# Kernel optimization log

Measured on AMD Instinct MI355X. Metric: run time of the kernel, lower is better.

The kernel has to match this reference:

```python
import jax, jax.numpy as jnp
import numpy as np

D_MODEL = 1024
D_FFN = 2048
WINDOW = 64
EPS = 1e-6


def rmsnorm(x, w):
    rms = jnp.sqrt(jnp.mean(x * x, axis=-1, keepdims=True) + EPS)
    return x / rms * w


def setup_inputs() -> dict:
    key = jax.random.key(0)
    ks = jax.random.split(key, 9)
    s = 0.02
    return {
        "x": jax.random.normal(ks[0], (4, 2048, D_MODEL), dtype=jnp.float32),
        "norm1_w": jnp.ones((D_MODEL,), dtype=jnp.float32),
        "norm2_w": jnp.ones((D_MODEL,), dtype=jnp.float32),
        "Wq": jax.random.normal(ks[1], (D_MODEL, D_MODEL), dtype=jnp.float32) * s,
        "Wk": jax.random.normal(ks[2], (D_MODEL, D_MODEL), dtype=jnp.float32) * s,
        "Wv": jax.random.normal(ks[3], (D_MODEL, D_MODEL), dtype=jnp.float32) * s,
        "Wo": jax.random.normal(ks[4], (D_MODEL, D_MODEL), dtype=jnp.float32) * s,
        "W1": jax.random.normal(ks[5], (D_MODEL, D_FFN), dtype=jnp.float32) * s,
        "W2": jax.random.normal(ks[6], (D_FFN, D_MODEL), dtype=jnp.float32) * s,
        "W3": jax.random.normal(ks[7], (D_MODEL, D_FFN), dtype=jnp.float32) * s,
    }


def reference(x, norm1_w, norm2_w, Wq, Wk, Wv, Wo, W1, W2, W3):
    B, T, D = x.shape
    scale = D ** (-0.5)
    residual = x
    xn = rmsnorm(x, norm1_w)
    q = xn @ Wq  # [B,T,D]
    k = xn @ Wk
    v = xn @ Wv
    # causal local-window mask: attend iff 0 <= i-j < WINDOW
    rows = jnp.arange(T)[:, None]
    cols = jnp.arange(T)[None, :]
    mask = (cols <= rows) & (rows - cols < WINDOW)  # [T,T] bool
    scores = jnp.einsum("bid,bjd->bij", q, k) * scale
    scores = jnp.where(mask[None], scores, -jnp.inf)
    weights = jax.nn.softmax(scores, axis=-1)
    attended = jnp.einsum("bij,bjd->bid", weights, v)
    x = residual + attended @ Wo
    # SwiGLU FFN
    xn2 = rmsnorm(x, norm2_w)
    ffn = (jax.nn.silu(xn2 @ W1) * (xn2 @ W3)) @ W2
    return x + ffn
```

## Files before the change

kernel.cpp:

```cpp
#include <hip/hip_runtime.h>
#include <hip/hip_bf16.h>

typedef __attribute__((ext_vector_type(8))) short bf16x8;
typedef __attribute__((ext_vector_type(4))) float f32x4;

__device__ __forceinline__ short to_bf16s(float f) {
    union { __hip_bfloat16 h; short s; } u;
    u.h = __float2bfloat16(f);
    return u.s;
}

__device__ __forceinline__ void load_lds16(const void* g, void* l) {
    __builtin_amdgcn_global_load_lds((const __attribute__((address_space(1))) void*)g,
                                     (__attribute__((address_space(3))) void*)l, 16, 0, 0);
}

__global__ __launch_bounds__(256)
void prep_kernel(const float* __restrict__ Wq, const float* __restrict__ Wk,
                 const float* __restrict__ Wv, const float* __restrict__ Wo,
                 const float* __restrict__ W1, const float* __restrict__ W3,
                 const float* __restrict__ W2,
                 short* __restrict__ WqT, short* __restrict__ WkT,
                 short* __restrict__ WvT, short* __restrict__ WoT,
                 short* __restrict__ W13T, short* __restrict__ W2T,
                 const float* __restrict__ x, const float* __restrict__ n1w,
                 short* __restrict__ xn1) {
    const int bid = blockIdx.x;
    const int t = threadIdx.x;
    if (bid >= 10240) {
        const long row = bid - 10240;
        float4 v = ((const float4*)(x + row * 1024))[t];
        float ss = v.x * v.x + v.y * v.y + v.z * v.z + v.w * v.w;
        #pragma unroll
        for (int off = 32; off; off >>= 1) ss += __shfl_xor(ss, off);
        __shared__ float red[4];
        if ((t & 63) == 0) red[t >> 6] = ss;
        __syncthreads();
        ss = red[0] + red[1] + red[2] + red[3];
        const float inv = rsqrtf(ss * (1.0f / 1024.0f) + 1e-6f);
        float4 wv = ((const float4*)n1w)[t];
        short4 o;
        o.x = to_bf16s(v.x * inv * wv.x);
        o.y = to_bf16s(v.y * inv * wv.y);
        o.z = to_bf16s(v.z * inv * wv.z);
        o.w = to_bf16s(v.w * inv * wv.w);
        *(short4*)&xn1[row * 1024 + t * 4] = o;
        return;
    }
    __shared__ float tile[32][33];
    const float* src; short* dst; int K, N, tl, rs = 1, ro = 0;
    if (bid < 4096) {
        const int wi = bid >> 10; tl = bid & 1023;
        src = wi == 0 ? Wq : wi == 1 ? Wk : wi == 2 ? Wv : Wo;
        dst = wi == 0 ? WqT : wi == 1 ? WkT : wi == 2 ? WvT : WoT;
        K = 1024; N = 1024;
    } else if (bid < 8192) {
        const int wi = (bid - 4096) >> 11; tl = (bid - 4096) & 2047;
        src = wi ? W3 : W1; dst = W13T; rs = 2; ro = wi;
        K = 1024; N = 2048;
    } else {
        tl = bid - 8192; src = W2; dst = W2T;
        K = 2048; N = 1024;
    }
    const int nx = N >> 5;
    const int n0 = (tl % nx) * 32, k0 = (tl / nx) * 32;
    {
        const int lr = t >> 3, lc = (t & 7) * 4;
        float4 v = *(const float4*)&src[(long)(k0 + lr) * N + n0 + lc];
        tile[lr][lc] = v.x; tile[lr][lc + 1] = v.y;
        tile[lr][lc + 2] = v.z; tile[lr][lc + 3] = v.w;
    }
    __syncthreads();
    {
        const int nr = t >> 3, kc = (t & 7) * 4;
        short4 o;
        o.x = to_bf16s(tile[kc][nr]);
        o.y = to_bf16s(tile[kc + 1][nr]);
        o.z = to_bf16s(tile[kc + 2][nr]);
        o.w = to_bf16s(tile[kc + 3][nr]);
        *(short4*)&dst[(long)((n0 + nr) * rs + ro) * K + k0 + kc] = o;
    }
}

__global__ __launch_bounds__(256)
void rmsnorm_kernel(const float* __restrict__ x, const float* __restrict__ wt,
                    short* __restrict__ out) {
    const long row = blockIdx.x;
    const int t = threadIdx.x;
    float4 v = ((const float4*)(x + row * 1024))[t];
    float ss = v.x * v.x + v.y * v.y + v.z * v.z + v.w * v.w;
    #pragma unroll
    for (int off = 32; off; off >>= 1) ss += __shfl_xor(ss, off);
    __shared__ float red[4];
    if ((t & 63) == 0) red[t >> 6] = ss;
    __syncthreads();
    ss = red[0] + red[1] + red[2] + red[3];
    const float inv = rsqrtf(ss * (1.0f / 1024.0f) + 1e-6f);
    float4 wv = ((const float4*)wt)[t];
    short4 o;
    o.x = to_bf16s(v.x * inv * wv.x);
    o.y = to_bf16s(v.y * inv * wv.y);
    o.z = to_bf16s(v.z * inv * wv.z);
    o.w = to_bf16s(v.w * inv * wv.w);
    *(short4*)&out[row * 1024 + t * 4] = o;
}

#define MFMA16(MB, NB, BREG)                                                   \
    __builtin_amdgcn_s_barrier();                                              \
    asm volatile("s_waitcnt lgkmcnt(0)");                                      \
    __builtin_amdgcn_s_setprio(1);                                             \
    _Pragma("unroll")                                                          \
    for (int m_ = 0; m_ < 4; ++m_)                                             \
        _Pragma("unroll")                                                      \
        for (int n_ = 0; n_ < 2; ++n_) {                                       \
            acc[(MB) + m_][(NB) + n_] = __builtin_amdgcn_mfma_f32_16x16x32_bf16( \
                a[m_][0], BREG[n_][0], acc[(MB) + m_][(NB) + n_], 0, 0, 0);    \
            acc[(MB) + m_][(NB) + n_] = __builtin_amdgcn_mfma_f32_16x16x32_bf16( \
                a[m_][1], BREG[n_][1], acc[(MB) + m_][(NB) + n_], 0, 0, 0);    \
        }                                                                      \
    __builtin_amdgcn_s_setprio(0);                                             \
    __builtin_amdgcn_s_barrier();

#define QRA(BUF)                                                               \
    _Pragma("unroll")                                                          \
    for (int m_ = 0; m_ < 4; ++m_) {                                           \
        const int rb_ = ((BUF) * 2 + (wr >> 1)) * 16384 +                      \
                        ((wr & 1) * 64 + m_ * 16 + lm) * 128;                  \
        a[m_][0] = *(const bf16x8*)&lds[rb_ + ((lk * 16) ^ sw)];               \
        a[m_][1] = *(const bf16x8*)&lds[rb_ + ((64 + lk * 16) ^ sw)];          \
    }
#define QRB(BUF, NG, ARR)                                                      \
    _Pragma("unroll")                                                          \
    for (int n_ = 0; n_ < 2; ++n_) {                                           \
        const int rb_ = 65536 + ((BUF) * 2 + wc) * 8192 +                      \
                        (((NG) * 2 + n_) * 16 + lm) * 128;                     \
        ARR[n_][0] = *(const bf16x8*)&lds[rb_ + ((lk * 16) ^ sw)];             \
        ARR[n_][1] = *(const bf16x8*)&lds[rb_ + ((64 + lk * 16) ^ sw)];        \
    }

__global__ __launch_bounds__(512, 2)
void gemm256qkv(const short* __restrict__ A, const short* __restrict__ B0,
                short* __restrict__ outp, short* __restrict__ outp2,
                int M, int N, int K) {
    __shared__ __align__(16) char lds[98304];

    const int t = threadIdx.x;
    const int lane = t & 63, w = t >> 6;
    const int wr = w >> 1, wc = w & 1;
    const int lm = lane & 15, lk = lane >> 4;
    const int sw = (lm & 7) << 4;

    const int nbn = N >> 7;
    const int chunk = gridDim.x >> 3;
    const int logical = (blockIdx.x & 7) * chunk + (blockIdx.x >> 3);
    const int bm = logical / nbn, bn = logical - (logical / nbn) * nbn;

    const long Kb = (long)K * 2;
    const char* Ab = (const char*)A;
    const char* Bb = (const char*)B0;

    long srcA[2][2], srcB[2];
    {
        const int rowp = t >> 3;
        const int cbx = (t & 7) * 16;
        const int swz = ((t >> 3) & 7) << 4;
        #pragma unroll
        for (int h = 0; h < 2; ++h)
            #pragma unroll
            for (int c = 0; c < 2; ++c)
                srcA[h][c] = (long)(bm * 256 + h * 128 + c * 64 + rowp) * Kb + (cbx ^ swz);
        #pragma unroll
        for (int h = 0; h < 2; ++h)
            srcB[h] = (long)(bn * 128 + h * 64 + rowp) * Kb + (cbx ^ swz);
    }
    auto stA = [&](int kt, int h) {
        const int buf = kt & 1;
        #pragma unroll
        for (int c = 0; c < 2; ++c)
            load_lds16(Ab + srcA[h][c] + (long)kt * 128,
                       &lds[(buf * 2 + h) * 16384 + c * 8192 + t * 16]);
    };
    auto stB = [&](int kt, int h) {
        const int buf = kt & 1;
        load_lds16(Bb + srcB[h] + (long)kt * 128,
                   &lds[65536 + (buf * 2 + h) * 8192 + t * 16]);
    };

    f32x4 acc[4][4] = {};
    bf16x8 a[4][2], b0[2][2], b1[2][2];
    const int nt = K >> 6;

    stA(0, 0); stA(0, 1); stB(0, 0); stB(0, 1);
    stA(1, 0); stA(1, 1); stB(1, 0); stB(1, 1);
    asm volatile("s_waitcnt vmcnt(6)" ::: "memory");
    __builtin_amdgcn_s_barrier();

    for (int u = 0; u < nt; u += 2) {
        const bool pf = (u + 2) < nt;
        QRA(0); QRB(0, 0, b0);
        if (pf) stA(u + 2, 0);
        MFMA16(0, 0, b0)
        QRB(0, 1, b1);
        if (pf) { stA(u + 2, 1); stB(u + 2, 0); stB(u + 2, 1);
                  asm volatile("s_waitcnt vmcnt(6)" ::: "memory"); }
        else    { asm volatile("s_waitcnt vmcnt(0)" ::: "memory"); }
        MFMA16(0, 2, b1)
        QRA(1); QRB(1, 0, b0);
        if (pf) stA(u + 3, 0);
        MFMA16(0, 0, b0)
        QRB(1, 1, b1);
        if (pf) { stA(u + 3, 1); stB(u + 3, 0); stB(u + 3, 1);
                  asm volatile("s_waitcnt vmcnt(6)" ::: "memory"); }
        else    { asm volatile("s_waitcnt vmcnt(0)" ::: "memory"); }
        MFMA16(0, 2, b1)
    }

    #pragma unroll
    for (int mf = 0; mf < 4; ++mf)
      #pragma unroll
      for (int nf = 0; nf < 4; ++nf)
        #pragma unroll
        for (int r = 0; r < 4; ++r) {
            const int grow = bm * 256 + wr * 64 + mf * 16 + lk * 4 + r;
            const int gcol = bn * 128 + wc * 64 + nf * 16 + lm;
            const float v = acc[mf][nf][r];
            if (gcol < 2048)
                outp[(long)grow * 2048 + gcol] = to_bf16s(v);
            else
                outp2[(long)(gcol - 2048) * 8192 + grow] = to_bf16s(v);
        }
}

__global__ __launch_bounds__(256, 2)
void gemm128o(const short* __restrict__ A, const short* __restrict__ B0,
              const float* __restrict__ res, float* __restrict__ outp,
              int M, int N, int K) {
    __shared__ __align__(16) char lds[65536];

    const int t = threadIdx.x;
    const int lane = t & 63, w = t >> 6;
    const int wr = w >> 1, wc = w & 1;
    const int lm = lane & 15, lk = lane >> 4;
    const int sw = (lm & 7) << 4;

    const int nbn = N >> 7;
    const int chunk = gridDim.x >> 3;
    const int logical = (blockIdx.x & 7) * chunk + (blockIdx.x >> 3);
    const int bm = logical / nbn, bn = logical - (logical / nbn) * nbn;

    const long Kb = (long)K * 2;
    const char* Ab = (const char*)A;
    const char* Bb = (const char*)B0;

    long srcA[4], srcB[4];
    {
        const int rowp = t >> 3;
        const int cbx = (t & 7) * 16;
        const int swz = ((t >> 3) & 7) << 4;
        #pragma unroll
        for (int c = 0; c < 4; ++c) {
            srcA[c] = (long)(bm * 128 + c * 32 + rowp) * Kb + (cbx ^ swz);
            srcB[c] = (long)(bn * 128 + c * 32 + rowp) * Kb + (cbx ^ swz);
        }
    }
    auto stage = [&](int kt, int buf) {
        #pragma unroll
        for (int c = 0; c < 4; ++c)
            load_lds16(Ab + srcA[c] + (long)kt * 128,
                       &lds[buf * 16384 + c * 4096 + t * 16]);
        #pragma unroll
        for (int c = 0; c < 4; ++c)
            load_lds16(Bb + srcB[c] + (long)kt * 128,
                       &lds[32768 + buf * 16384 + c * 4096 + t * 16]);
    };

    f32x4 acc[4][4] = {};
    const int nt = K >> 6;

    stage(0, 0);
    asm volatile("s_waitcnt vmcnt(0)" ::: "memory");
    __syncthreads();

    for (int kt = 0; kt < nt; ++kt) {
        const int buf = kt & 1;
        if (kt + 1 < nt) stage(kt + 1, buf ^ 1);
        bf16x8 a[4][2], b[4][2];
        #pragma unroll
        for (int m = 0; m < 4; ++m) {
            const int rb = buf * 16384 + (wr * 64 + m * 16 + lm) * 128;
            a[m][0] = *(const bf16x8*)&lds[rb + ((lk * 16) ^ sw)];
            a[m][1] = *(const bf16x8*)&lds[rb + ((64 + lk * 16) ^ sw)];
        }
        #pragma unroll
        for (int n = 0; n < 4; ++n) {
            const int rb = 32768 + buf * 16384 + (wc * 64 + n * 16 + lm) * 128;
            b[n][0] = *(const bf16x8*)&lds[rb + ((lk * 16) ^ sw)];
            b[n][1] = *(const bf16x8*)&lds[rb + ((64 + lk * 16) ^ sw)];
        }
        #pragma unroll
        for (int m = 0; m < 4; ++m)
            #pragma unroll
            for (int n = 0; n < 4; ++n) {
                acc[m][n] = __builtin_amdgcn_mfma_f32_16x16x32_bf16(a[m][0], b[n][0], acc[m][n], 0, 0, 0);
                acc[m][n] = __builtin_amdgcn_mfma_f32_16x16x32_bf16(a[m][1], b[n][1], acc[m][n], 0, 0, 0);
            }
        __syncthreads();
    }

    #pragma unroll
    for (int m = 0; m < 4; ++m)
      #pragma unroll
      for (int n = 0; n < 4; ++n)
        #pragma unroll
        for (int r = 0; r < 4; ++r) {
            const int grow = bm * 128 + wr * 64 + m * 16 + lk * 4 + r;
            const int gcol = bn * 128 + wc * 64 + n * 16 + lm;
            const long i = (long)grow * N + gcol;
            outp[i] = res[i] + acc[m][n][r];
        }
}

#define RA2(BUF, MG)                                                           \
    _Pragma("unroll")                                                          \
    for (int m_ = 0; m_ < 4; ++m_) {                                           \
        const int rb_ = ((BUF) * 2 + wr) * 16384 + (((MG) * 4 + m_) * 16 + lm) * 128; \
        a[m_][0] = *(const bf16x8*)&lds[rb_ + ((lk * 16) ^ sw)];               \
        a[m_][1] = *(const bf16x8*)&lds[rb_ + ((64 + lk * 16) ^ sw)];          \
    }
#define RB2(BUF, NH, ARR)                                                      \
    _Pragma("unroll")                                                          \
    for (int n_ = 0; n_ < 2; ++n_) {                                           \
        const int rb_ = 65536 + ((BUF) * 2 + (wc >> 1)) * 16384 +              \
                        ((wc & 1) * 64 + ((NH) * 2 + n_) * 16 + lm) * 128;     \
        ARR[n_][0] = *(const bf16x8*)&lds[rb_ + ((lk * 16) ^ sw)];             \
        ARR[n_][1] = *(const bf16x8*)&lds[rb_ + ((64 + lk * 16) ^ sw)];        \
    }

__global__ __launch_bounds__(512, 2)
void gemm256f(const short* __restrict__ A, const short* __restrict__ B0,
              short* __restrict__ outp, int M, int N, int K) {
    __shared__ __align__(16) char lds[131072];

    const int t = threadIdx.x;
    const int lane = t & 63, w = t >> 6;
    const int wr = w >> 2, wc = w & 3;
    const int lm = lane & 15, lk = lane >> 4;
    const int sw = (lm & 7) << 4;

    const int nbn = N >> 8;
    const int chunk = gridDim.x >> 3;
    const int logical = (blockIdx.x & 7) * chunk + (blockIdx.x >> 3);
    const int bm = logical / nbn, bn = logical - (logical / nbn) * nbn;

    const long Kb = (long)K * 2;
    const char* Ab = (const char*)A;
    const char* Bb = (const char*)B0;

    long srcA[2][2], srcB[2][2];
    {
        const int rowp = t >> 3;
        const int cbx = (t & 7) * 16;
        const int swz = ((t >> 3) & 7) << 4;
        #pragma unroll
        for (int h = 0; h < 2; ++h)
            #pragma unroll
            for (int c = 0; c < 2; ++c) {
                srcA[h][c] = (long)(bm * 256 + h * 128 + c * 64 + rowp) * Kb + (cbx ^ swz);
                srcB[h][c] = (long)(bn * 256 + h * 128 + c * 64 + rowp) * Kb + (cbx ^ swz);
            }
    }
    auto stA = [&](int kt, int h) {
        const int buf = kt & 1;
        #pragma unroll
        for (int c = 0; c < 2; ++c)
            load_lds16(Ab + srcA[h][c] + (long)kt * 128,
                       &lds[(buf * 2 + h) * 16384 + c * 8192 + t * 16]);
    };
    auto stB = [&](int kt, int h) {
        const int buf = kt & 1;
        #pragma unroll
        for (int c = 0; c < 2; ++c)
            load_lds16(Bb + srcB[h][c] + (long)kt * 128,
                       &lds[65536 + (buf * 2 + h) * 16384 + c * 8192 + t * 16]);
    };

    f32x4 acc[8][4] = {};
    bf16x8 a[4][2], b0[2][2], b1[2][2];
    const int nt = K >> 6;

    stB(0, 0); stB(0, 1); stA(0, 0); stA(0, 1); stB(1, 0); stB(1, 1);
    asm volatile("s_waitcnt vmcnt(4)" ::: "memory");
    __builtin_amdgcn_s_barrier();

    for (int u = 0; u < nt; u += 2) {
        const bool pf = (u + 2) < nt;
        RA2(0, 0); RB2(0, 0, b0);
        stA(u + 1, 0);
        MFMA16(0, 0, b0)
        RB2(0, 1, b1);
        stA(u + 1, 1);
        MFMA16(0, 2, b1)
        RA2(0, 1);
        if (pf) stB(u + 2, 0);
        MFMA16(4, 2, b1)
        if (pf) { stB(u + 2, 1); asm volatile("s_waitcnt vmcnt(4)" ::: "memory"); }
        else    { asm volatile("s_waitcnt vmcnt(0)" ::: "memory"); }
        MFMA16(4, 0, b0)
        RA2(1, 0); RB2(1, 0, b0);
        if (pf) stA(u + 2, 0);
        MFMA16(0, 0, b0)
        RB2(1, 1, b1);
        if (pf) stA(u + 2, 1);
        MFMA16(0, 2, b1)
        RA2(1, 1);
        if (pf) stB(u + 3, 0);
        MFMA16(4, 2, b1)
        if (pf) { stB(u + 3, 1); asm volatile("s_waitcnt vmcnt(4)" ::: "memory"); }
        else    { asm volatile("s_waitcnt vmcnt(0)" ::: "memory"); }
        MFMA16(4, 0, b0)
    }

    const int NH = N >> 1;
    #pragma unroll
    for (int mf = 0; mf < 8; ++mf)
      #pragma unroll
      for (int nf = 0; nf < 4; ++nf)
        #pragma unroll
        for (int r = 0; r < 4; ++r) {
            const int grow = bm * 256 + wr * 128 + mf * 16 + lk * 4 + r;
            const int gcol = bn * 256 + wc * 64 + nf * 16 + lm;
            const float v = acc[mf][nf][r];
            const float g3 = __shfl_xor(v, 1);
            if (!(lane & 1)) {
                const float sws = v / (1.f + __expf(-v));
                outp[(long)grow * NH + (gcol >> 1)] = to_bf16s(sws * g3);
            }
        }
}

__global__ __launch_bounds__(128)
void attn_kernel(const short* __restrict__ Q, const short* __restrict__ Km,
                 int ldq, const short* __restrict__ VT, short* __restrict__ att) {
    const int T = 2048, D = 1024, Mtot = 8192;
    const int bid = blockIdx.x;
    const int b = bid >> 6;
    const int q0 = (bid & 63) << 5;
    const long qrow0 = (long)b * T + q0;
    const int t = threadIdx.x, lane = t & 63, w = t >> 6;

    __shared__ short Qs[2][32 * 32];
    __shared__ short Ks[2][96 * 32];
    __shared__ float S_lds[32][100];
    __shared__ short P_lds[32 * 96];
    __shared__ short VTs[2][128 * 96];

    const int trow = t >> 2, tk8 = (t & 3) * 8;
    auto stageQK = [&](int kt, int bf) {
        const int k0 = kt << 5;
        load_lds16(Q + (qrow0 + trow) * ldq + k0 + tk8, &Qs[bf][t * 8]);
        #pragma unroll
        for (int s2 = 0; s2 < 3; ++s2) {
            const int krow = s2 * 32 + trow;
            int j = q0 - 64 + krow; if (j < 0) j = 0;
            load_lds16(Km + ((long)b * T + j) * ldq + k0 + tk8, &Ks[bf][(s2 * 128 + t) * 8]);
        }
    };

    f32x4 s[6] = {};
    stageQK(0, 0);
    __syncthreads();
    for (int kt = 0; kt < 32; ++kt) {
        const int cb = kt & 1;
        if (kt + 1 < 32) stageQK(kt + 1, cb ^ 1);
        const int ko = (lane >> 4) * 8;
        const bf16x8 aq = *(const bf16x8*)&Qs[cb][(w * 16 + (lane & 15)) * 32 + ko];
        #pragma unroll
        for (int n = 0; n < 6; ++n) {
            const bf16x8 bk = *(const bf16x8*)&Ks[cb][(n * 16 + (lane & 15)) * 32 + ko];
            s[n] = __builtin_amdgcn_mfma_f32_16x16x32_bf16(aq, bk, s[n], 0, 0, 0);
        }
        __syncthreads();
    }
    #pragma unroll
    for (int n = 0; n < 6; ++n)
        #pragma unroll
        for (int r = 0; r < 4; ++r)
            S_lds[w * 16 + ((lane >> 4) << 2) + r][n * 16 + (lane & 15)] = s[n][r] * 0.03125f;
    __syncthreads();

    {
        const int row = t >> 2, c0 = (t & 3) * 24;
        float e[24];
        float mx = -1e30f;
        #pragma unroll
        for (int c = 0; c < 24; ++c) {
            const int kj = c0 + c;
            const bool valid = (kj > row) && (kj <= row + 64) && (q0 - 64 + kj >= 0);
            const float sv = valid ? S_lds[row][kj] : -1e30f;
            e[c] = sv;
            mx = fmaxf(mx, sv);
        }
        mx = fmaxf(mx, __shfl_xor(mx, 1));
        mx = fmaxf(mx, __shfl_xor(mx, 2));
        float sum = 0.f;
        #pragma unroll
        for (int c = 0; c < 24; ++c) {
            const float ev = (e[c] > -1e29f) ? __expf(e[c] - mx) : 0.f;
            e[c] = ev; sum += ev;
        }
        sum += __shfl_xor(sum, 1);
        sum += __shfl_xor(sum, 2);
        const float inv = 1.f / sum;
        #pragma unroll
        for (int c = 0; c < 24; ++c)
            P_lds[row * 96 + c0 + c] = to_bf16s(e[c] * inv);
    }

    auto stageV = [&](int dc, int bf) {
        #pragma unroll
        for (int s2 = 0; s2 < 12; ++s2) {
            const int idx = s2 * 128 + t;
            const int dr = idx / 12, c = idx - dr * 12;
            int j = q0 - 64 + c * 8; if (j < 0) j = 0;
            load_lds16(VT + (long)(dc * 128 + dr) * Mtot + b * T + j, &VTs[bf][idx * 8]);
        }
    };
    stageV(0, 0);
    __syncthreads();

    bf16x8 pa[3];
    {
        const int ko = (lane >> 4) * 8;
        #pragma unroll
        for (int kc = 0; kc < 3; ++kc)
            pa[kc] = *(const bf16x8*)&P_lds[(w * 16 + (lane & 15)) * 96 + kc * 32 + ko];
    }
    for (int dc = 0; dc < 8; ++dc) {
        const int cb = dc & 1;
        if (dc + 1 < 8) stageV(dc + 1, cb ^ 1);
        f32x4 o[8] = {};
        const int ko = (lane >> 4) * 8;
        #pragma unroll
        for (int kc = 0; kc < 3; ++kc)
            #pragma unroll
            for (int n = 0; n < 8; ++n) {
                const bf16x8 vb = *(const bf16x8*)&VTs[cb][(n * 16 + (lane & 15)) * 96 + kc * 32 + ko];
                o[n] = __builtin_amdgcn_mfma_f32_16x16x32_bf16(pa[kc], vb, o[n], 0, 0, 0);
            }
        __syncthreads();
        #pragma unroll
        for (int n = 0; n < 8; ++n)
            #pragma unroll
            for (int r = 0; r < 4; ++r) {
                const long grow = qrow0 + w * 16 + ((lane >> 4) << 2) + r;
                const int gcol = dc * 128 + n * 16 + (lane & 15);
                att[grow * D + gcol] = to_bf16s(o[n][r]);
            }
    }
}

extern "C" void kernel_launch(void* const* d_in, const int* in_sizes, int n_in,
                              void* d_out, int out_size, void* d_ws, size_t ws_size,
                              hipStream_t stream) {
    const float* x   = (const float*)d_in[0];
    const float* n1w = (const float*)d_in[1];
    const float* n2w = (const float*)d_in[2];
    const float* Wq  = (const float*)d_in[3];
    const float* Wk  = (const float*)d_in[4];
    const float* Wv  = (const float*)d_in[5];
    const float* Wo  = (const float*)d_in[6];
    const float* W1  = (const float*)d_in[7];
    const float* W2  = (const float*)d_in[8];
    const float* W3  = (const float*)d_in[9];

    const int M = 8192;
    char* ws = (char*)d_ws;
    size_t off = 0;
    auto alloc = [&](size_t bytes) { void* p = ws + off; off += (bytes + 255) & ~(size_t)255; return p; };

    short* xn1 = (short*)alloc((size_t)M * 1024 * 2);
    short* qk  = (short*)alloc((size_t)M * 2048 * 2);
    short* vT  = (short*)alloc((size_t)M * 1024 * 2);
    float* x2  = (float*)alloc((size_t)M * 1024 * 4);
    short* WqT = (short*)alloc((size_t)1024 * 1024 * 2);
    short* WkT = (short*)alloc((size_t)1024 * 1024 * 2);
    short* WvT = (short*)alloc((size_t)1024 * 1024 * 2);
    short* WoT = (short*)alloc((size_t)1024 * 1024 * 2);
    short* W13T= (short*)alloc((size_t)4096 * 1024 * 2);
    short* W2T = (short*)alloc((size_t)1024 * 2048 * 2);
    short* att = xn1;
    short* xn2 = qk;
    short* h   = qk + (size_t)M * 1024;

    prep_kernel<<<18432, 256, 0, stream>>>(Wq, Wk, Wv, Wo, W1, W3, W2,
                                           WqT, WkT, WvT, WoT, W13T, W2T,
                                           x, n1w, xn1);
    gemm256qkv<<<768, 512, 0, stream>>>(xn1, WqT, qk, vT, M, 3072, 1024);
    attn_kernel<<<256, 128, 0, stream>>>(qk, qk + 1024, 2048, vT, att);
    gemm128o<<<512, 256, 0, stream>>>(att, WoT, x, x2, M, 1024, 1024);
    rmsnorm_kernel<<<M, 256, 0, stream>>>(x2, n2w, xn2);
    gemm256f<<<512, 512, 0, stream>>>(xn2, W13T, h, M, 4096, 1024);
    gemm128o<<<512, 256, 0, stream>>>(h, W2T, x2, (float*)d_out, M, 1024, 2048);
}
```

Measured before the change: 299.2 us.

## Retile all GEMMs with simpler single-barrier double-buffered loops and larger tiles

The QKV GEMM moves to 256x192 tiles with 8 waves in a 2x4 layout, giving 512 blocks instead of 768. The two residual GEMMs move from 128x128 tiles with 256 threads to 256x128 tiles with 512 threads. The SwiGLU GEMM and all the others drop the hand-interleaved half-step MFMA/prefetch schedule for a plain per-k-tile double-buffer loop with one barrier and a full vmcnt(0) wait. Larger tiles raise data reuse and cut block count, but the simpler schedule may overlap loads with MFMA less well, and the grids may leave some CUs idle.

```diff
diff --git a/kernel.cpp b/kernel.cpp
--- a/kernel.cpp
+++ b/kernel.cpp
@@ -105,52 +105,20 @@
     *(short4*)&out[row * 1024 + t * 4] = o;
 }
 
-#define MFMA16(MB, NB, BREG)                                                   \
-    __builtin_amdgcn_s_barrier();                                              \
-    asm volatile("s_waitcnt lgkmcnt(0)");                                      \
-    __builtin_amdgcn_s_setprio(1);                                             \
-    _Pragma("unroll")                                                          \
-    for (int m_ = 0; m_ < 4; ++m_)                                             \
-        _Pragma("unroll")                                                      \
-        for (int n_ = 0; n_ < 2; ++n_) {                                       \
-            acc[(MB) + m_][(NB) + n_] = __builtin_amdgcn_mfma_f32_16x16x32_bf16( \
-                a[m_][0], BREG[n_][0], acc[(MB) + m_][(NB) + n_], 0, 0, 0);    \
-            acc[(MB) + m_][(NB) + n_] = __builtin_amdgcn_mfma_f32_16x16x32_bf16( \
-                a[m_][1], BREG[n_][1], acc[(MB) + m_][(NB) + n_], 0, 0, 0);    \
-        }                                                                      \
-    __builtin_amdgcn_s_setprio(0);                                             \
-    __builtin_amdgcn_s_barrier();
-
-#define QRA(BUF)                                                               \
-    _Pragma("unroll")                                                          \
-    for (int m_ = 0; m_ < 4; ++m_) {                                           \
-        const int rb_ = ((BUF) * 2 + (wr >> 1)) * 16384 +                      \
-                        ((wr & 1) * 64 + m_ * 16 + lm) * 128;                  \
-        a[m_][0] = *(const bf16x8*)&lds[rb_ + ((lk * 16) ^ sw)];               \
-        a[m_][1] = *(const bf16x8*)&lds[rb_ + ((64 + lk * 16) ^ sw)];          \
-    }
-#define QRB(BUF, NG, ARR)                                                      \
-    _Pragma("unroll")                                                          \
-    for (int n_ = 0; n_ < 2; ++n_) {                                           \
-        const int rb_ = 65536 + ((BUF) * 2 + wc) * 8192 +                      \
-                        (((NG) * 2 + n_) * 16 + lm) * 128;                     \
-        ARR[n_][0] = *(const bf16x8*)&lds[rb_ + ((lk * 16) ^ sw)];             \
-        ARR[n_][1] = *(const bf16x8*)&lds[rb_ + ((64 + lk * 16) ^ sw)];        \
-    }
 
 __global__ __launch_bounds__(512, 2)
-void gemm256qkv(const short* __restrict__ A, const short* __restrict__ B0,
+void gemm192qkv(const short* __restrict__ A, const short* __restrict__ B0,
                 short* __restrict__ outp, short* __restrict__ outp2,
                 int M, int N, int K) {
-    __shared__ __align__(16) char lds[98304];
+    __shared__ __align__(16) char lds[114688];
 
     const int t = threadIdx.x;
     const int lane = t & 63, w = t >> 6;
-    const int wr = w >> 1, wc = w & 1;
+    const int wr = w >> 2, wc = w & 3;
     const int lm = lane & 15, lk = lane >> 4;
     const int sw = (lm & 7) << 4;
 
-    const int nbn = N >> 7;
+    const int nbn = N / 192;
     const int chunk = gridDim.x >> 3;
     const int logical = (blockIdx.x & 7) * chunk + (blockIdx.x >> 3);
     const int bm = logical / nbn, bn = logical - (logical / nbn) * nbn;
@@ -159,70 +127,88 @@
     const char* Ab = (const char*)A;
     const char* Bb = (const char*)B0;
 
-    long srcA[2][2], srcB[2];
+    long srcA[4], srcB[3];
     {
         const int rowp = t >> 3;
         const int cbx = (t & 7) * 16;
         const int swz = ((t >> 3) & 7) << 4;
         #pragma unroll
-        for (int h = 0; h < 2; ++h)
-            #pragma unroll
-            for (int c = 0; c < 2; ++c)
-                srcA[h][c] = (long)(bm * 256 + h * 128 + c * 64 + rowp) * Kb + (cbx ^ swz);
-        #pragma unroll
-        for (int h = 0; h < 2; ++h)
-            srcB[h] = (long)(bn * 128 + h * 64 + rowp) * Kb + (cbx ^ swz);
-    }
-    auto stA = [&](int kt, int h) {
+        for (int c = 0; c < 4; ++c)
+            srcA[c] = (long)(bm * 256 + c * 64 + rowp) * Kb + (cbx ^ swz);
+        #pragma unroll
+        for (int c = 0; c < 3; ++c)
+            srcB[c] = (long)(bn * 192 + c * 64 + rowp) * Kb + (cbx ^ swz);
+    }
+    auto stage = [&](int kt) {
         const int buf = kt & 1;
         #pragma unroll
-        for (int c = 0; c < 2; ++c)
-            load_lds16(Ab + srcA[h][c] + (long)kt * 128,
-                       &lds[(buf * 2 + h) * 16384 + c * 8192 + t * 16]);
+        for (int c = 0; c < 4; ++c)
+            load_lds16(Ab + srcA[c] + (long)kt * 128, &lds[buf * 32768 + c * 8192 + t * 16]);
+        #pragma unroll
+        for (int c = 0; c < 3; ++c)
+            load_lds16(Bb + srcB[c] + (long)kt * 128, &lds[65536 + buf * 24576 + c * 8192 + t * 16]);
     };
-    auto stB = [&](int kt, int h) {
+
+    f32x4 acc[8][3] = {};
+    bf16x8 a[4][2], b[3][2];
+    const int nt = K >> 6;
+
+    stage(0);
+    asm volatile("s_waitcnt vmcnt(0)" ::: "memory");
+    __builtin_amdgcn_s_barrier();
+
+    for (int kt = 0; kt < nt; ++kt) {
         const int buf = kt & 1;
-        load_lds16(Bb + srcB[h] + (long)kt * 128,
-                   &lds[65536 + (buf * 2 + h) * 8192 + t * 16]);
-    };
-
-    f32x4 acc[4][4] = {};
-    bf16x8 a[4][2], b0[2][2], b1[2][2];
-    const int nt = K >> 6;
-
-    stA(0, 0); stA(0, 1); stB(0, 0); stB(0, 1);
-    stA(1, 0); stA(1, 1); stB(1, 0); stB(1, 1);
-    asm volatile("s_waitcnt vmcnt(6)" ::: "memory");
-    __builtin_amdgcn_s_barrier();
-
-    for (int u = 0; u < nt; u += 2) {
-        const bool pf = (u + 2) < nt;
-        QRA(0); QRB(0, 0, b0);
-        if (pf) stA(u + 2, 0);
-        MFMA16(0, 0, b0)
-        QRB(0, 1, b1);
-        if (pf) { stA(u + 2, 1); stB(u + 2, 0); stB(u + 2, 1);
-                  asm volatile("s_waitcnt vmcnt(6)" ::: "memory"); }
-        else    { asm volatile("s_waitcnt vmcnt(0)" ::: "memory"); }
-        MFMA16(0, 2, b1)
-        QRA(1); QRB(1, 0, b0);
-        if (pf) stA(u + 3, 0);
-        MFMA16(0, 0, b0)
-        QRB(1, 1, b1);
-        if (pf) { stA(u + 3, 1); stB(u + 3, 0); stB(u + 3, 1);
-                  asm volatile("s_waitcnt vmcnt(6)" ::: "memory"); }
-        else    { asm volatile("s_waitcnt vmcnt(0)" ::: "memory"); }
-        MFMA16(0, 2, b1)
+        const bool pf = kt + 1 < nt;
+        #pragma unroll
+        for (int n_ = 0; n_ < 3; ++n_) {
+            const int rb = 65536 + buf * 24576 + (wc * 48 + n_ * 16 + lm) * 128;
+            b[n_][0] = *(const bf16x8*)&lds[rb + ((lk * 16) ^ sw)];
+            b[n_][1] = *(const bf16x8*)&lds[rb + ((64 + lk * 16) ^ sw)];
+        }
+        #pragma unroll
+        for (int m_ = 0; m_ < 4; ++m_) {
+            const int rb = buf * 32768 + (wr * 128 + m_ * 16 + lm) * 128;
+            a[m_][0] = *(const bf16x8*)&lds[rb + ((lk * 16) ^ sw)];
+            a[m_][1] = *(const bf16x8*)&lds[rb + ((64 + lk * 16) ^ sw)];
+        }
+        if (pf) stage(kt + 1);
+        asm volatile("s_waitcnt lgkmcnt(0)");
+        __builtin_amdgcn_s_setprio(1);
+        #pragma unroll
+        for (int m_ = 0; m_ < 4; ++m_)
+            #pragma unroll
+            for (int n_ = 0; n_ < 3; ++n_) {
+                acc[m_][n_] = __builtin_amdgcn_mfma_f32_16x16x32_bf16(a[m_][0], b[n_][0], acc[m_][n_], 0, 0, 0);
+                acc[m_][n_] = __builtin_amdgcn_mfma_f32_16x16x32_bf16(a[m_][1], b[n_][1], acc[m_][n_], 0, 0, 0);
+            }
+        #pragma unroll
+        for (int m_ = 0; m_ < 4; ++m_) {
+            const int rb = buf * 32768 + (wr * 128 + 64 + m_ * 16 + lm) * 128;
+            a[m_][0] = *(const bf16x8*)&lds[rb + ((lk * 16) ^ sw)];
+            a[m_][1] = *(const bf16x8*)&lds[rb + ((64 + lk * 16) ^ sw)];
+        }
+        asm volatile("s_waitcnt lgkmcnt(0)");
+        #pragma unroll
+        for (int m_ = 0; m_ < 4; ++m_)
+            #pragma unroll
+            for (int n_ = 0; n_ < 3; ++n_) {
+                acc[4 + m_][n_] = __builtin_amdgcn_mfma_f32_16x16x32_bf16(a[m_][0], b[n_][0], acc[4 + m_][n_], 0, 0, 0);
+                acc[4 + m_][n_] = __builtin_amdgcn_mfma_f32_16x16x32_bf16(a[m_][1], b[n_][1], acc[4 + m_][n_], 0, 0, 0);
+            }
+        __builtin_amdgcn_s_setprio(0);
+        if (pf) asm volatile("s_waitcnt vmcnt(0)" ::: "memory");
+        __builtin_amdgcn_s_barrier();
     }
 
     #pragma unroll
-    for (int mf = 0; mf < 4; ++mf)
+    for (int mf = 0; mf < 8; ++mf)
       #pragma unroll
-      for (int nf = 0; nf < 4; ++nf)
+      for (int nf = 0; nf < 3; ++nf)
         #pragma unroll
         for (int r = 0; r < 4; ++r) {
-            const int grow = bm * 256 + wr * 64 + mf * 16 + lk * 4 + r;
-            const int gcol = bn * 128 + wc * 64 + nf * 16 + lm;
+            const int grow = bm * 256 + wr * 128 + mf * 16 + lk * 4 + r;
+            const int gcol = bn * 192 + wc * 48 + nf * 16 + lm;
             const float v = acc[mf][nf][r];
             if (gcol < 2048)
                 outp[(long)grow * 2048 + gcol] = to_bf16s(v);
@@ -231,114 +217,9 @@
         }
 }
 
-__global__ __launch_bounds__(256, 2)
-void gemm128o(const short* __restrict__ A, const short* __restrict__ B0,
-              const float* __restrict__ res, float* __restrict__ outp,
-              int M, int N, int K) {
-    __shared__ __align__(16) char lds[65536];
-
-    const int t = threadIdx.x;
-    const int lane = t & 63, w = t >> 6;
-    const int wr = w >> 1, wc = w & 1;
-    const int lm = lane & 15, lk = lane >> 4;
-    const int sw = (lm & 7) << 4;
-
-    const int nbn = N >> 7;
-    const int chunk = gridDim.x >> 3;
-    const int logical = (blockIdx.x & 7) * chunk + (blockIdx.x >> 3);
-    const int bm = logical / nbn, bn = logical - (logical / nbn) * nbn;
-
-    const long Kb = (long)K * 2;
-    const char* Ab = (const char*)A;
-    const char* Bb = (const char*)B0;
-
-    long srcA[4], srcB[4];
-    {
-        const int rowp = t >> 3;
-        const int cbx = (t & 7) * 16;
-        const int swz = ((t >> 3) & 7) << 4;
-        #pragma unroll
-        for (int c = 0; c < 4; ++c) {
-            srcA[c] = (long)(bm * 128 + c * 32 + rowp) * Kb + (cbx ^ swz);
-            srcB[c] = (long)(bn * 128 + c * 32 + rowp) * Kb + (cbx ^ swz);
-        }
-    }
-    auto stage = [&](int kt, int buf) {
-        #pragma unroll
-        for (int c = 0; c < 4; ++c)
-            load_lds16(Ab + srcA[c] + (long)kt * 128,
-                       &lds[buf * 16384 + c * 4096 + t * 16]);
-        #pragma unroll
-        for (int c = 0; c < 4; ++c)
-            load_lds16(Bb + srcB[c] + (long)kt * 128,
-                       &lds[32768 + buf * 16384 + c * 4096 + t * 16]);
-    };
-
-    f32x4 acc[4][4] = {};
-    const int nt = K >> 6;
-
-    stage(0, 0);
-    asm volatile("s_waitcnt vmcnt(0)" ::: "memory");
-    __syncthreads();
-
-    for (int kt = 0; kt < nt; ++kt) {
-        const int buf = kt & 1;
-        if (kt + 1 < nt) stage(kt + 1, buf ^ 1);
-        bf16x8 a[4][2], b[4][2];
-        #pragma unroll
-        for (int m = 0; m < 4; ++m) {
-            const int rb = buf * 16384 + (wr * 64 + m * 16 + lm) * 128;
-            a[m][0] = *(const bf16x8*)&lds[rb + ((lk * 16) ^ sw)];
-            a[m][1] = *(const bf16x8*)&lds[rb + ((64 + lk * 16) ^ sw)];
-        }
-        #pragma unroll
-        for (int n = 0; n < 4; ++n) {
-            const int rb = 32768 + buf * 16384 + (wc * 64 + n * 16 + lm) * 128;
-            b[n][0] = *(const bf16x8*)&lds[rb + ((lk * 16) ^ sw)];
-            b[n][1] = *(const bf16x8*)&lds[rb + ((64 + lk * 16) ^ sw)];
-        }
-        #pragma unroll
-        for (int m = 0; m < 4; ++m)
-            #pragma unroll
-            for (int n = 0; n < 4; ++n) {
-                acc[m][n] = __builtin_amdgcn_mfma_f32_16x16x32_bf16(a[m][0], b[n][0], acc[m][n], 0, 0, 0);
-                acc[m][n] = __builtin_amdgcn_mfma_f32_16x16x32_bf16(a[m][1], b[n][1], acc[m][n], 0, 0, 0);
-            }
-        __syncthreads();
-    }
-
-    #pragma unroll
-    for (int m = 0; m < 4; ++m)
-      #pragma unroll
-      for (int n = 0; n < 4; ++n)
-        #pragma unroll
-        for (int r = 0; r < 4; ++r) {
-            const int grow = bm * 128 + wr * 64 + m * 16 + lk * 4 + r;
-            const int gcol = bn * 128 + wc * 64 + n * 16 + lm;
-            const long i = (long)grow * N + gcol;
-            outp[i] = res[i] + acc[m][n][r];
-        }
-}
-
-#define RA2(BUF, MG)                                                           \
-    _Pragma("unroll")                                                          \
-    for (int m_ = 0; m_ < 4; ++m_) {                                           \
-        const int rb_ = ((BUF) * 2 + wr) * 16384 + (((MG) * 4 + m_) * 16 + lm) * 128; \
-        a[m_][0] = *(const bf16x8*)&lds[rb_ + ((lk * 16) ^ sw)];               \
-        a[m_][1] = *(const bf16x8*)&lds[rb_ + ((64 + lk * 16) ^ sw)];          \
-    }
-#define RB2(BUF, NH, ARR)                                                      \
-    _Pragma("unroll")                                                          \
-    for (int n_ = 0; n_ < 2; ++n_) {                                           \
-        const int rb_ = 65536 + ((BUF) * 2 + (wc >> 1)) * 16384 +              \
-                        ((wc & 1) * 64 + ((NH) * 2 + n_) * 16 + lm) * 128;     \
-        ARR[n_][0] = *(const bf16x8*)&lds[rb_ + ((lk * 16) ^ sw)];             \
-        ARR[n_][1] = *(const bf16x8*)&lds[rb_ + ((64 + lk * 16) ^ sw)];        \
-    }
-
 __global__ __launch_bounds__(512, 2)
-void gemm256f(const short* __restrict__ A, const short* __restrict__ B0,
-              short* __restrict__ outp, int M, int N, int K) {
+void gemm256fv2(const short* __restrict__ A, const short* __restrict__ B0,
+                short* __restrict__ outp, int M, int N, int K) {
     __shared__ __align__(16) char lds[131072];
 
     const int t = threadIdx.x;
@@ -356,68 +237,77 @@
     const char* Ab = (const char*)A;
     const char* Bb = (const char*)B0;
 
-    long srcA[2][2], srcB[2][2];
+    long srcA[4], srcB[4];
     {
         const int rowp = t >> 3;
         const int cbx = (t & 7) * 16;
         const int swz = ((t >> 3) & 7) << 4;
         #pragma unroll
-        for (int h = 0; h < 2; ++h)
-            #pragma unroll
-            for (int c = 0; c < 2; ++c) {
-                srcA[h][c] = (long)(bm * 256 + h * 128 + c * 64 + rowp) * Kb + (cbx ^ swz);
-                srcB[h][c] = (long)(bn * 256 + h * 128 + c * 64 + rowp) * Kb + (cbx ^ swz);
-            }
-    }
-    auto stA = [&](int kt, int h) {
+        for (int c = 0; c < 4; ++c) {
+            srcA[c] = (long)(bm * 256 + c * 64 + rowp) * Kb + (cbx ^ swz);
+            srcB[c] = (long)(bn * 256 + c * 64 + rowp) * Kb + (cbx ^ swz);
+        }
+    }
+    auto stage = [&](int kt) {
         const int buf = kt & 1;
         #pragma unroll
-        for (int c = 0; c < 2; ++c)
-            load_lds16(Ab + srcA[h][c] + (long)kt * 128,
-                       &lds[(buf * 2 + h) * 16384 + c * 8192 + t * 16]);
+        for (int c = 0; c < 4; ++c)
+            load_lds16(Ab + srcA[c] + (long)kt * 128, &lds[buf * 32768 + c * 8192 + t * 16]);
+        #pragma unroll
+        for (int c = 0; c < 4; ++c)
+            load_lds16(Bb + srcB[c] + (long)kt * 128, &lds[65536 + buf * 32768 + c * 8192 + t * 16]);
     };
-    auto stB = [&](int kt, int h) {
+
+    f32x4 acc[8][4] = {};
+    bf16x8 a[4][2], b[4][2];
+    const int nt = K >> 6;
+
+    stage(0);
+    asm volatile("s_waitcnt vmcnt(0)" ::: "memory");
+    __builtin_amdgcn_s_barrier();
+
+    for (int kt = 0; kt < nt; ++kt) {
         const int buf = kt & 1;
-        #pragma unroll
-        for (int c = 0; c < 2; ++c)
-            load_lds16(Bb + srcB[h][c] + (long)kt * 128,
-                       &lds[65536 + (buf * 2 + h) * 16384 + c * 8192 + t * 16]);
-    };
-
-    f32x4 acc[8][4] = {};
-    bf16x8 a[4][2], b0[2][2], b1[2][2];
-    const int nt = K >> 6;
-
-    stB(0, 0); stB(0, 1); stA(0, 0); stA(0, 1); stB(1, 0); stB(1, 1);
-    asm volatile("s_waitcnt vmcnt(4)" ::: "memory");
-    __builtin_amdgcn_s_barrier();
-
-    for (int u = 0; u < nt; u += 2) {
-        const bool pf = (u + 2) < nt;
-        RA2(0, 0); RB2(0, 0, b0);
-        stA(u + 1, 0);
-        MFMA16(0, 0, b0)
-        RB2(0, 1, b1);
-        stA(u + 1, 1);
-        MFMA16(0, 2, b1)
-        RA2(0, 1);
-        if (pf) stB(u + 2, 0);
-        MFMA16(4, 2, b1)
-        if (pf) { stB(u + 2, 1); asm volatile("s_waitcnt vmcnt(4)" ::: "memory"); }
-        else    { asm volatile("s_waitcnt vmcnt(0)" ::: "memory"); }
-        MFMA16(4, 0, b0)
-        RA2(1, 0); RB2(1, 0, b0);
-        if (pf) stA(u + 2, 0);
-        MFMA16(0, 0, b0)
-        RB2(1, 1, b1);
-        if (pf) stA(u + 2, 1);
-        MFMA16(0, 2, b1)
-        RA2(1, 1);
-        if (pf) stB(u + 3, 0);
-        MFMA16(4, 2, b1)
-        if (pf) { stB(u + 3, 1); asm volatile("s_waitcnt vmcnt(4)" ::: "memory"); }
-        else    { asm volatile("s_waitcnt vmcnt(0)" ::: "memory"); }
-        MFMA16(4, 0, b0)
+        const bool pf = kt + 1 < nt;
+        #pragma unroll
+        for (int n_ = 0; n_ < 4; ++n_) {
+            const int rb = 65536 + buf * 32768 + (wc * 64 + n_ * 16 + lm) * 128;
+            b[n_][0] = *(const bf16x8*)&lds[rb + ((lk * 16) ^ sw)];
+            b[n_][1] = *(const bf16x8*)&lds[rb + ((64 + lk * 16) ^ sw)];
+        }
+        #pragma unroll
+        for (int m_ = 0; m_ < 4; ++m_) {
+            const int rb = buf * 32768 + (wr * 128 + m_ * 16 + lm) * 128;
+            a[m_][0] = *(const bf16x8*)&lds[rb + ((lk * 16) ^ sw)];
+            a[m_][1] = *(const bf16x8*)&lds[rb + ((64 + lk * 16) ^ sw)];
+        }
+        if (pf) stage(kt + 1);
+        asm volatile("s_waitcnt lgkmcnt(0)");
+        __builtin_amdgcn_s_setprio(1);
+        #pragma unroll
+        for (int m_ = 0; m_ < 4; ++m_)
+            #pragma unroll
+            for (int n_ = 0; n_ < 4; ++n_) {
+                acc[m_][n_] = __builtin_amdgcn_mfma_f32_16x16x32_bf16(a[m_][0], b[n_][0], acc[m_][n_], 0, 0, 0);
+                acc[m_][n_] = __builtin_amdgcn_mfma_f32_16x16x32_bf16(a[m_][1], b[n_][1], acc[m_][n_], 0, 0, 0);
+            }
+        #pragma unroll
+        for (int m_ = 0; m_ < 4; ++m_) {
+            const int rb = buf * 32768 + (wr * 128 + 64 + m_ * 16 + lm) * 128;
+            a[m_][0] = *(const bf16x8*)&lds[rb + ((lk * 16) ^ sw)];
+            a[m_][1] = *(const bf16x8*)&lds[rb + ((64 + lk * 16) ^ sw)];
+        }
+        asm volatile("s_waitcnt lgkmcnt(0)");
+        #pragma unroll
+        for (int m_ = 0; m_ < 4; ++m_)
+            #pragma unroll
+            for (int n_ = 0; n_ < 4; ++n_) {
+                acc[4 + m_][n_] = __builtin_amdgcn_mfma_f32_16x16x32_bf16(a[m_][0], b[n_][0], acc[4 + m_][n_], 0, 0, 0);
+                acc[4 + m_][n_] = __builtin_amdgcn_mfma_f32_16x16x32_bf16(a[m_][1], b[n_][1], acc[4 + m_][n_], 0, 0, 0);
+            }
+        __builtin_amdgcn_s_setprio(0);
+        if (pf) asm volatile("s_waitcnt vmcnt(0)" ::: "memory");
+        __builtin_amdgcn_s_barrier();
     }
 
     const int NH = N >> 1;
@@ -435,6 +325,100 @@
                 const float sws = v / (1.f + __expf(-v));
                 outp[(long)grow * NH + (gcol >> 1)] = to_bf16s(sws * g3);
             }
+        }
+}
+
+__global__ __launch_bounds__(512, 2)
+void gemm128res(const short* __restrict__ A, const short* __restrict__ B0,
+                const float* __restrict__ res, float* __restrict__ outp,
+                int M, int N, int K) {
+    __shared__ __align__(16) char lds[98304];
+
+    const int t = threadIdx.x;
+    const int lane = t & 63, w = t >> 6;
+    const int wr = w >> 1, wc = w & 1;
+    const int lm = lane & 15, lk = lane >> 4;
+    const int sw = (lm & 7) << 4;
+
+    const int nbn = N >> 7;
+    const int chunk = gridDim.x >> 3;
+    const int logical = (blockIdx.x & 7) * chunk + (blockIdx.x >> 3);
+    const int bm = logical / nbn, bn = logical - (logical / nbn) * nbn;
+
+    const long Kb = (long)K * 2;
+    const char* Ab = (const char*)A;
+    const char* Bb = (const char*)B0;
+
+    long srcA[4], srcB[2];
+    {
+        const int rowp = t >> 3;
+        const int cbx = (t & 7) * 16;
+        const int swz = ((t >> 3) & 7) << 4;
+        #pragma unroll
+        for (int c = 0; c < 4; ++c)
+            srcA[c] = (long)(bm * 256 + c * 64 + rowp) * Kb + (cbx ^ swz);
+        #pragma unroll
+        for (int c = 0; c < 2; ++c)
+            srcB[c] = (long)(bn * 128 + c * 64 + rowp) * Kb + (cbx ^ swz);
+    }
+    auto stage = [&](int kt) {
+        const int buf = kt & 1;
+        #pragma unroll
+        for (int c = 0; c < 4; ++c)
+            load_lds16(Ab + srcA[c] + (long)kt * 128, &lds[buf * 32768 + c * 8192 + t * 16]);
+        #pragma unroll
+        for (int c = 0; c < 2; ++c)
+            load_lds16(Bb + srcB[c] + (long)kt * 128, &lds[65536 + buf * 16384 + c * 8192 + t * 16]);
+    };
+
+    f32x4 acc[4][4] = {};
+    bf16x8 a[4][2], b[4][2];
+    const int nt = K >> 6;
+
+    stage(0);
+    asm volatile("s_waitcnt vmcnt(0)" ::: "memory");
+    __builtin_amdgcn_s_barrier();
+
+    for (int kt = 0; kt < nt; ++kt) {
+        const int buf = kt & 1;
+        const bool pf = kt + 1 < nt;
+        #pragma unroll
+        for (int m_ = 0; m_ < 4; ++m_) {
+            const int rb = buf * 32768 + (wr * 64 + m_ * 16 + lm) * 128;
+            a[m_][0] = *(const bf16x8*)&lds[rb + ((lk * 16) ^ sw)];
+            a[m_][1] = *(const bf16x8*)&lds[rb + ((64 + lk * 16) ^ sw)];
+        }
+        #pragma unroll
+        for (int n_ = 0; n_ < 4; ++n_) {
+            const int rb = 65536 + buf * 16384 + (wc * 64 + n_ * 16 + lm) * 128;
+            b[n_][0] = *(const bf16x8*)&lds[rb + ((lk * 16) ^ sw)];
+            b[n_][1] = *(const bf16x8*)&lds[rb + ((64 + lk * 16) ^ sw)];
+        }
+        if (pf) stage(kt + 1);
+        asm volatile("s_waitcnt lgkmcnt(0)");
+        __builtin_amdgcn_s_setprio(1);
+        #pragma unroll
+        for (int m_ = 0; m_ < 4; ++m_)
+            #pragma unroll
+            for (int n_ = 0; n_ < 4; ++n_) {
+                acc[m_][n_] = __builtin_amdgcn_mfma_f32_16x16x32_bf16(a[m_][0], b[n_][0], acc[m_][n_], 0, 0, 0);
+                acc[m_][n_] = __builtin_amdgcn_mfma_f32_16x16x32_bf16(a[m_][1], b[n_][1], acc[m_][n_], 0, 0, 0);
+            }
+        __builtin_amdgcn_s_setprio(0);
+        if (pf) asm volatile("s_waitcnt vmcnt(0)" ::: "memory");
+        __builtin_amdgcn_s_barrier();
+    }
+
+    #pragma unroll
+    for (int mf = 0; mf < 4; ++mf)
+      #pragma unroll
+      for (int nf = 0; nf < 4; ++nf)
+        #pragma unroll
+        for (int r = 0; r < 4; ++r) {
+            const int grow = bm * 256 + wr * 64 + mf * 16 + lk * 4 + r;
+            const int gcol = bn * 128 + wc * 64 + nf * 16 + lm;
+            const long i = (long)grow * N + gcol;
+            outp[i] = res[i] + acc[mf][nf][r];
         }
 }
 
@@ -595,10 +579,10 @@
     prep_kernel<<<18432, 256, 0, stream>>>(Wq, Wk, Wv, Wo, W1, W3, W2,
                                            WqT, WkT, WvT, WoT, W13T, W2T,
                                            x, n1w, xn1);
-    gemm256qkv<<<768, 512, 0, stream>>>(xn1, WqT, qk, vT, M, 3072, 1024);
+    gemm192qkv<<<512, 512, 0, stream>>>(xn1, WqT, qk, vT, M, 3072, 1024);
     attn_kernel<<<256, 128, 0, stream>>>(qk, qk + 1024, 2048, vT, att);
-    gemm128o<<<512, 256, 0, stream>>>(att, WoT, x, x2, M, 1024, 1024);
+    gemm128res<<<256, 512, 0, stream>>>(att, WoT, x, x2, M, 1024, 1024);
     rmsnorm_kernel<<<M, 256, 0, stream>>>(x2, n2w, xn2);
-    gemm256f<<<512, 512, 0, stream>>>(xn2, W13T, h, M, 4096, 1024);
-    gemm128o<<<512, 256, 0, stream>>>(h, W2T, x2, (float*)d_out, M, 1024, 2048);
-}
+    gemm256fv2<<<512, 512, 0, stream>>>(xn2, W13T, h, M, 4096, 1024);
+    gemm128res<<<256, 512, 0, stream>>>(h, W2T, x2, (float*)d_out, M, 1024, 2048);
+}
```

Measured after the change: 310.4 us. +3.7%, slower.
